# Performance work log

Hardware: AMD Instinct MI355X
Metric: run time of the kernel (lower is better)

## Reference

```python
import jax, jax.numpy as jnp
import numpy as np

B, S, E, H = 2, 2048, 1024, 16
D = E // H  # head_dim = 64


def setup_inputs() -> dict:
    key = jax.random.key(0)
    ks = jax.random.split(key, 6)
    scale = 1.0 / np.sqrt(E)
    x = jax.random.normal(ks[0], (B, S, E), dtype=jnp.float32)
    mask = jnp.ones((B, S), dtype=jnp.int32)
    Wqkv = jax.random.normal(ks[1], (E, 3 * E), dtype=jnp.float32) * scale
    bqkv = jax.random.normal(ks[2], (3 * E,), dtype=jnp.float32) * 0.01
    Wout = jax.random.normal(ks[3], (E, E), dtype=jnp.float32) * scale
    bout = jax.random.normal(ks[4], (E,), dtype=jnp.float32) * 0.01
    return {"x": x, "mask": mask, "Wqkv": Wqkv, "bqkv": bqkv, "Wout": Wout, "bout": bout}


def reference(x, mask, Wqkv, bqkv, Wout, bout):
    Bn, Sn, En = x.shape
    qkv = x @ Wqkv + bqkv                      # [B,S,3E]
    qkv = qkv.reshape(Bn, Sn, 3, H, D)
    qkv = jnp.transpose(qkv, (2, 0, 3, 1, 4))  # [3,B,H,S,D]
    q, k, v = qkv[0], qkv[1], qkv[2]
    scores = jnp.einsum('bhqd,bhkd->bhqk', q, k) / np.sqrt(D).astype(np.float32)
    m = mask[:, None, None, :]                 # [B,1,1,S]
    scores = jnp.where(m == 0, jnp.float32(-jnp.inf), scores)
    attn = jax.nn.softmax(scores, axis=-1)
    out = jnp.einsum('bhqk,bhkd->bhqd', attn, v)  # [B,H,S,D]
    out = jnp.transpose(out, (0, 2, 1, 3)).reshape(Bn, Sn, En)
    return out @ Wout + bout
```

## Files before the change

### kernel.cpp

```cpp
#include <hip/hip_runtime.h>


typedef __attribute__((ext_vector_type(8))) short short8;
typedef __attribute__((ext_vector_type(4))) short short4b;
typedef __attribute__((ext_vector_type(4))) float floatx4;
typedef __attribute__((ext_vector_type(16))) float floatx16;
typedef unsigned short ushort_t;

static __device__ __forceinline__ ushort_t f2bf(float f) {
    unsigned u = __float_as_uint(f);
    u += 0x7fffu + ((u >> 16) & 1u);
    return (ushort_t)(u >> 16);
}
static __device__ __forceinline__ float bf2f(ushort_t h) {
    return __uint_as_float(((unsigned)h) << 16);
}
#if __has_builtin(__builtin_amdgcn_cvt_pk_bf16_f32)
typedef __attribute__((ext_vector_type(2))) __bf16 bf16x2_t;
static __device__ __forceinline__ unsigned pack2bf(float a, float b) {
    bf16x2_t r = __builtin_amdgcn_cvt_pk_bf16_f32(a, b);
    return __builtin_bit_cast(unsigned, r);
}
#else
static __device__ __forceinline__ unsigned pack2bf(float a, float b) {
    return (unsigned)f2bf(a) | ((unsigned)f2bf(b) << 16);
}
#endif
static __device__ __forceinline__ float hexp2(float x) {
    return __builtin_amdgcn_exp2f(x);
}
static __device__ __forceinline__ void gload16(const void* g, void* l) {
    __builtin_amdgcn_global_load_lds(
        (const __attribute__((address_space(1))) unsigned int*)g,
        (__attribute__((address_space(3))) unsigned int*)l, 16, 0, 0);
}

#if __has_builtin(__builtin_amdgcn_permlane32_swap)
typedef __attribute__((ext_vector_type(2))) unsigned uint2v_t;
static __device__ __forceinline__ void plswap(unsigned x, unsigned y,
                                              unsigned& o0, unsigned& o1) {
    uint2v_t r = __builtin_amdgcn_permlane32_swap(x, y, false, false);
    o0 = r.x; o1 = r.y;
}
#else
static __device__ __forceinline__ void plswap(unsigned x, unsigned y,
                                              unsigned& o0, unsigned& o1) {
    int l = (int)(threadIdx.x & 63);
    bool hi = l >= 32;
    unsigned xsw = (unsigned)__shfl((int)x, l ^ 32);
    unsigned ysw = (unsigned)__shfl((int)y, l ^ 32);
    o0 = hi ? ysw : x;
    o1 = hi ? y : xsw;
}
#endif

__global__ __launch_bounds__(256) void prep(
    const float* __restrict__ x, ushort_t* __restrict__ xb,
    const float* __restrict__ Wqkv, ushort_t* __restrict__ wqT,
    const float* __restrict__ Wout, ushort_t* __restrict__ woT,
    const int* __restrict__ mask, float* __restrict__ maddg)
{
    __shared__ float tile[32][33];
    const int bk = blockIdx.x;
    const int t = threadIdx.x;
    if (bk < 4096) {
        int i = bk * 256 + t;
        float4 v = ((const float4*)x)[i];
        uint2 o;
        o.x = pack2bf(v.x, v.y);
        o.y = pack2bf(v.z, v.w);
        ((uint2*)xb)[i] = o;
        return;
    }
    if (bk < 8192) {
        const float* W; ushort_t* WT; int K, N, id;
        if (bk < 7168) { W = Wqkv; WT = wqT; K = 1024; N = 3072; id = bk - 4096;
                         int nb = (id % 96) * 32, kb = (id / 96) * 32;
                         const int r = t >> 3, c4 = (t & 7) * 4;
                         float4 v = *(const float4*)&W[(size_t)(kb + r) * N + nb + c4];
                         tile[r][c4+0]=v.x; tile[r][c4+1]=v.y; tile[r][c4+2]=v.z; tile[r][c4+3]=v.w;
                         __syncthreads();
                         uint2 o;
                         o.x = pack2bf(tile[c4+0][r], tile[c4+1][r]);
                         o.y = pack2bf(tile[c4+2][r], tile[c4+3][r]);
                         ((uint2*)WT)[((size_t)(nb + r) * K + kb + c4) >> 2] = o;
        } else {         W = Wout; WT = woT; K = 1024; N = 1024; id = bk - 7168;
                         int nb = (id % 32) * 32, kb = (id / 32) * 32;
                         const int r = t >> 3, c4 = (t & 7) * 4;
                         float4 v = *(const float4*)&W[(size_t)(kb + r) * N + nb + c4];
                         tile[r][c4+0]=v.x; tile[r][c4+1]=v.y; tile[r][c4+2]=v.z; tile[r][c4+3]=v.w;
                         __syncthreads();
                         uint2 o;
                         o.x = pack2bf(tile[c4+0][r], tile[c4+1][r]);
                         o.y = pack2bf(tile[c4+2][r], tile[c4+3][r]);
                         ((uint2*)WT)[((size_t)(nb + r) * K + kb + c4) >> 2] = o;
        }
        return;
    }
    {
        int i = (bk - 8192) * 256 + t;
        maddg[i] = (mask[i] ? 0.f : -1e30f) - 24.0f;
    }
}

__global__ __launch_bounds__(256, 3) void gemm_qkv(
    const ushort_t* __restrict__ A, const ushort_t* __restrict__ B,
    const float* __restrict__ bias, ushort_t* __restrict__ qkvb,
    ushort_t* __restrict__ vtg)
{
    const int K = 1024;
    __shared__ ushort_t Ah[128][32], Bh[128][32];
    __shared__ ushort_t Tb[64][136];
    const int bn = blockIdx.x * 128, bm = blockIdx.y * 128;
    const int t = threadIdx.x, w = t >> 6, lane = t & 63;
    const int l15 = lane & 15, quad = lane >> 4;
    const int wm = w >> 1, wn = w & 1;

    const int srow = w * 32 + (lane >> 2);
    const int skp  = (lane & 3) ^ ((lane >> 2) & 3);
    const int scol = skp * 8;
    const ushort_t* ga = A + (size_t)(bm + srow) * K + scol;
    const ushort_t* gb = B + (size_t)(bn + srow) * K + scol;
    const size_t rstep = (size_t)16 * K;
    const int fcol = ((quad ^ (l15 & 3)) * 8);

    floatx4 acc[4][4];
    #pragma unroll
    for (int mt = 0; mt < 4; ++mt)
        #pragma unroll
        for (int nt = 0; nt < 4; ++nt) acc[mt][nt] = (floatx4){0.f, 0.f, 0.f, 0.f};

    for (int k0 = 0; k0 < K; k0 += 32) {
        #pragma unroll
        for (int i = 0; i < 2; ++i) {
            gload16(ga + i * rstep + k0, &Ah[w * 32 + i * 16][0]);
            gload16(gb + i * rstep + k0, &Bh[w * 32 + i * 16][0]);
        }
        __syncthreads();
        short8 ah[4], bh[4];
        #pragma unroll
        for (int x = 0; x < 4; ++x) {
            ah[x] = *(const short8*)&Ah[wm * 64 + x * 16 + l15][fcol];
            bh[x] = *(const short8*)&Bh[wn * 64 + x * 16 + l15][fcol];
        }
        #pragma unroll
        for (int mt = 0; mt < 4; ++mt)
            #pragma unroll
            for (int nt = 0; nt < 4; ++nt)
                acc[mt][nt] = __builtin_amdgcn_mfma_f32_16x16x32_bf16(ah[mt], bh[nt], acc[mt][nt], 0, 0, 0);
        __syncthreads();
    }

    if (bn < 2048) {
        #pragma unroll
        for (int mt = 0; mt < 4; ++mt)
            #pragma unroll
            for (int r = 0; r < 4; ++r) {
                size_t row = (size_t)(bm + wm * 64 + mt * 16 + quad * 4 + r) * 2048;
                #pragma unroll
                for (int nt = 0; nt < 4; ++nt) {
                    int col = bn + wn * 64 + nt * 16 + l15;
                    qkvb[row + col] = f2bf(acc[mt][nt][r] + bias[col]);
                }
            }
    } else {
        const int h0 = (bn - 2048) >> 6;
        const int b  = bm >> 11, s0 = bm & 2047;
        #pragma unroll
        for (int hh = 0; hh < 2; ++hh) {
            if (wn == hh) {
                #pragma unroll
                for (int mt = 0; mt < 4; ++mt)
                    #pragma unroll
                    for (int nt = 0; nt < 4; ++nt) {
                        int d = nt * 16 + l15;
                        int sb = wm * 64 + mt * 16 + quad * 4;
                        float bv = bias[bn + hh * 64 + nt * 16 + l15];
                        uint2 pk;
                        pk.x = pack2bf(acc[mt][nt][0] + bv, acc[mt][nt][1] + bv);
                        pk.y = pack2bf(acc[mt][nt][2] + bv, acc[mt][nt][3] + bv);
                        *(uint2*)&Tb[d][sb] = pk;
                    }
            }
            __syncthreads();
            ushort_t* vbase = vtg + ((size_t)((b * 16 + h0 + hh) * 64)) * 2048 + s0;
            #pragma unroll
            for (int it = 0; it < 4; ++it) {
                int idx = t + it * 256;
                int d = idx >> 4, ch = idx & 15;
                uint4 v = *(const uint4*)&Tb[d][ch * 8];
                *(uint4*)&vbase[(size_t)d * 2048 + ch * 8] = v;
            }
            __syncthreads();
        }
    }
}

__global__ __launch_bounds__(256, 3) void gemm_bf16_f32_64(
    const ushort_t* __restrict__ A, const ushort_t* __restrict__ B,
    const float* __restrict__ bias, float* __restrict__ C,
    int M, int N, int K)
{
    __shared__ ushort_t Ah[64][32], Bh[128][32];
    const int bn = blockIdx.x * 128, bm = blockIdx.y * 64;
    const int t = threadIdx.x, w = t >> 6, lane = t & 63;
    const int l15 = lane & 15, quad = lane >> 4;
    const int wm = w >> 1, wn = w & 1;

    const int srow = w * 16 + (lane >> 2);
    const int skp  = (lane & 3) ^ ((lane >> 2) & 3);
    const int scol = skp * 8;
    const ushort_t* ga  = A + (size_t)(bm + srow) * K + scol;
    const ushort_t* gb0 = B + (size_t)(bn + srow) * K + scol;
    const ushort_t* gb1 = B + (size_t)(bn + 64 + srow) * K + scol;
    const int fcol = ((quad ^ (l15 & 3)) * 8);

    floatx4 acc[2][4];
    #pragma unroll
    for (int mt = 0; mt < 2; ++mt)
        #pragma unroll
        for (int nt = 0; nt < 4; ++nt) acc[mt][nt] = (floatx4){0.f, 0.f, 0.f, 0.f};

    for (int k0 = 0; k0 < K; k0 += 32) {
        gload16(ga  + k0, &Ah[w * 16][0]);
        gload16(gb0 + k0, &Bh[w * 16][0]);
        gload16(gb1 + k0, &Bh[64 + w * 16][0]);
        __syncthreads();
        short8 ah[2], bh[4];
        #pragma unroll
        for (int x = 0; x < 2; ++x)
            ah[x] = *(const short8*)&Ah[wm * 32 + x * 16 + l15][fcol];
        #pragma unroll
        for (int x = 0; x < 4; ++x)
            bh[x] = *(const short8*)&Bh[wn * 64 + x * 16 + l15][fcol];
        #pragma unroll
        for (int mt = 0; mt < 2; ++mt)
            #pragma unroll
            for (int nt = 0; nt < 4; ++nt)
                acc[mt][nt] = __builtin_amdgcn_mfma_f32_16x16x32_bf16(ah[mt], bh[nt], acc[mt][nt], 0, 0, 0);
        __syncthreads();
    }
    #pragma unroll
    for (int mt = 0; mt < 2; ++mt)
        #pragma unroll
        for (int r = 0; r < 4; ++r) {
            size_t row = (size_t)(bm + wm * 32 + mt * 16 + quad * 4 + r) * N;
            #pragma unroll
            for (int nt = 0; nt < 4; ++nt) {
                int col = bn + wn * 64 + nt * 16 + l15;
                C[row + col] = acc[mt][nt][r] + bias[col];
            }
        }
}

__global__ __launch_bounds__(512)
__attribute__((amdgpu_waves_per_eu(4, 4)))
void flash_v13(
    const ushort_t* __restrict__ qkv, const ushort_t* __restrict__ vtg,
    const float* __restrict__ maddg, ushort_t* __restrict__ attn)
{
    __shared__ __align__(16) ushort_t Ks[2][2][64][64];
    __shared__ __align__(16) ushort_t Vt[2][2][64][64];

    const int blk = blockIdx.x;
    const int xcd = blk & 7, rr = blk >> 3;
    const int qi = rr & 15, g = xcd + 8 * (rr >> 4);
    const int b = g >> 4, h = g & 15, q0 = qi * 128;

    const int t = threadIdx.x, wave = t >> 6, lane = t & 63;
    const int half = wave >> 2, wsub = wave & 3;
    const int l31 = lane & 31, hi = lane >> 5, l7 = lane & 7;
    const size_t bS = (size_t)b * 2048;
    const float c1 = 0.125f * 1.44269504088896340736f;

    short8 qf[4];
    {
        int q = q0 + wsub * 32 + l31;
        const ushort_t* qp = qkv + (bS + q) * 2048 + h * 64 + hi * 8;
        #pragma unroll
        for (int ks = 0; ks < 4; ++ks)
            qf[ks] = *(const short8*)(qp + ks * 16);
    }

    const int srow  = wsub * 16 + (lane >> 3);
    const int schnk = ((lane & 7) ^ ((lane >> 3) & 7)) * 8;
    const ushort_t* gK = qkv + (bS + half * 1024 + srow) * 2048 + 1024 + h * 64 + schnk;
    const ushort_t* gV = vtg + ((size_t)(b * 16 + h) * 64 + srow) * 2048 + half * 1024 + schnk;
    const float* gM = maddg + b * 2048 + half * 1024;

    auto stageK = [&](int buf, int kkt) {
        const ushort_t* p = gK + (size_t)(kkt * 64) * 2048;
        gload16(p,            &Ks[half][buf][wsub * 16][0]);
        gload16(p + 8 * 2048, &Ks[half][buf][wsub * 16 + 8][0]);
    };
    auto stageV = [&](int buf, int kkt) {
        gload16(gV + kkt * 64,            &Vt[half][buf][wsub * 16][0]);
        gload16(gV + kkt * 64 + 8 * 2048, &Vt[half][buf][wsub * 16 + 8][0]);
    };

    floatx16 outacc[2] = {};
    float lsum = 0.f;

    auto QKSM = [&](int kkt, int kb, unsigned (&Wd)[2][4][2]) {
        const int k0 = kkt * 64;
        #pragma unroll
        for (int t32 = 0; t32 < 2; ++t32) {
            floatx16 sc = {};
            __builtin_amdgcn_s_setprio(1);
            #pragma unroll
            for (int ks = 0; ks < 4; ++ks) {
                const int ch = ((2 * ks + hi) ^ l7) * 8;
                short8 ka = *(const short8*)&Ks[half][kb][t32 * 32 + l31][ch];
                sc = __builtin_amdgcn_mfma_f32_32x32x16_bf16(ka, qf[ks], sc, 0, 0, 0);
            }
            __builtin_amdgcn_s_setprio(0);
            #pragma unroll
            for (int gr = 0; gr < 4; ++gr) {
                float4 m4 = *(const float4*)&gM[k0 + t32 * 32 + gr * 8 + hi * 4];
                float p0 = hexp2(fmaf(sc[gr * 4 + 0], c1, m4.x));
                float p1 = hexp2(fmaf(sc[gr * 4 + 1], c1, m4.y));
                float p2 = hexp2(fmaf(sc[gr * 4 + 2], c1, m4.z));
                float p3 = hexp2(fmaf(sc[gr * 4 + 3], c1, m4.w));
                lsum += (p0 + p1) + (p2 + p3);
                Wd[t32][gr][0] = pack2bf(p0, p1);
                Wd[t32][gr][1] = pack2bf(p2, p3);
            }
        }
    };
    auto PV = [&](int vb, unsigned (&Wd)[2][4][2]) {
        #pragma unroll
        for (int ks2 = 0; ks2 < 4; ++ks2) {
            const int t32 = ks2 >> 1;
            const int ae  = (ks2 & 1) * 2;
            uint4 u;
            plswap(Wd[t32][ae][0], Wd[t32][ae + 1][0], u.x, u.z);
            plswap(Wd[t32][ae][1], Wd[t32][ae + 1][1], u.y, u.w);
            short8 pb = __builtin_bit_cast(short8, u);
            const int ch = ((2 * ks2 + hi) ^ l7) * 8;
            __builtin_amdgcn_s_setprio(1);
            #pragma unroll
            for (int dt = 0; dt < 2; ++dt) {
                short8 va = *(const short8*)&Vt[half][vb][dt * 32 + l31][ch];
                outacc[dt] = __builtin_amdgcn_mfma_f32_32x32x16_bf16(va, pb, outacc[dt], 0, 0, 0);
            }
            __builtin_amdgcn_s_setprio(0);
        }
    };

    stageK(0, 0);
    stageK(1, 1);
    stageV(0, 0);
    __syncthreads();
    unsigned Wc[2][4][2];
    QKSM(0, 0, Wc);
    __syncthreads();

    for (int kt = 0; kt < 16; ++kt) {
        if (kt + 2 < 16) stageK(kt & 1, kt + 2);
        if (kt + 1 < 16) stageV((kt + 1) & 1, kt + 1);
        unsigned Wn[2][4][2];
        if (kt + 1 < 16) QKSM(kt + 1, (kt + 1) & 1, Wn);
        PV(kt & 1, Wc);
        __syncthreads();
        if (kt + 1 < 16) {
            #pragma unroll
            for (int i = 0; i < 2; ++i)
                #pragma unroll
                for (int j = 0; j < 4; ++j) {
                    Wc[i][j][0] = Wn[i][j][0];
                    Wc[i][j][1] = Wn[i][j][1];
                }
        }
    }

    lsum += __shfl_xor(lsum, 32);

    float* Obuf = (float*)&Ks[0][0][0][0];
    float* Lbuf = (float*)&Vt[0][0][0][0];

    if (half == 1) {
        #pragma unroll
        for (int dt = 0; dt < 2; ++dt)
            #pragma unroll
            for (int i = 0; i < 16; ++i)
                Obuf[(wsub * 64 + lane) * 32 + ((dt * 16 + i) ^ l31)] = outacc[dt][i];
        Lbuf[wsub * 32 + l31] = lsum;
    }
    __syncthreads();
    if (half == 0) {
        float inv = 1.f / (lsum + Lbuf[wsub * 32 + l31]);
        int q = q0 + wsub * 32 + l31;
        ushort_t* orow = attn + (bS + q) * 1024 + h * 64;
        #pragma unroll
        for (int dt = 0; dt < 2; ++dt) {
            float o[16];
            #pragma unroll
            for (int i = 0; i < 16; ++i)
                o[i] = outacc[dt][i] + Obuf[(wsub * 64 + lane) * 32 + ((dt * 16 + i) ^ l31)];
            #pragma unroll
            for (int gr = 0; gr < 4; ++gr) {
                uint2 pk;
                pk.x = pack2bf(o[gr * 4 + 0] * inv, o[gr * 4 + 1] * inv);
                pk.y = pack2bf(o[gr * 4 + 2] * inv, o[gr * 4 + 3] * inv);
                *(uint2*)&orow[dt * 32 + gr * 8 + hi * 4] = pk;
            }
        }
    }
}

extern "C" void kernel_launch(void* const* d_in, const int* in_sizes, int n_in,
                              void* d_out, int out_size, void* d_ws, size_t ws_size,
                              hipStream_t stream) {
    const float* x    = (const float*)d_in[0];
    const int*   mask = (const int*)  d_in[1];
    const float* Wqkv = (const float*)d_in[2];
    const float* bqkv = (const float*)d_in[3];
    const float* Wout = (const float*)d_in[4];
    const float* bout = (const float*)d_in[5];
    float* out = (float*)d_out;

    char* ws = (char*)d_ws;
    ushort_t* xb    = (ushort_t*)(ws);
    ushort_t* wqT   = (ushort_t*)(ws + 8388608);
    ushort_t* qkvb  = (ushort_t*)(ws + 14680064);
    ushort_t* vtg   = (ushort_t*)(ws + 31457280);
    ushort_t* attnb = (ushort_t*)(ws + 39845888);
    ushort_t* woT   = (ushort_t*)(ws + 48234496);
    float*    maddg = (float*)   (ws + 50331648);

    const int M = 4096, E = 1024, N3 = 3072;

    prep<<<dim3(8208), dim3(256), 0, stream>>>(
        x, xb, Wqkv, wqT, Wout, woT, mask, maddg);

    gemm_qkv<<<dim3(N3 / 128, M / 128), dim3(256), 0, stream>>>(
        xb, wqT, bqkv, qkvb, vtg);

    flash_v13<<<dim3(512), dim3(512), 0, stream>>>(qkvb, vtg, maddg, attnb);

    gemm_bf16_f32_64<<<dim3(E / 128, M / 64), dim3(256), 0, stream>>>(
        attnb, woT, bout, out, M, E, E);
}
```

Baseline: 205.7 us.

## Interleave QK-softmax and PV at 32-key granularity with unrolled double-buffer loop

Splits the QK/softmax and PV stages into 32-key halves and interleaves them, so each PV MFMA pair is scheduled next to the next tile's QK MFMA work. The P fragments are packed into MFMA operands right after exponentiation, which removes the per-iteration register copy of the unnormalised weights. The main loop is unrolled by two with fixed buffer indices, removing modulo buffer selection. This may raise register pressure under the fixed waves-per-EU setting and only reshapes the flash kernel, which is one of four launches.

```diff
diff --git a/kernel.cpp b/kernel.cpp
--- a/kernel.cpp
+++ b/kernel.cpp
@@ -255,7 +255,7 @@
 
 __global__ __launch_bounds__(512)
 __attribute__((amdgpu_waves_per_eu(4, 4)))
-void flash_v13(
+void flash_v14(
     const ushort_t* __restrict__ qkv, const ushort_t* __restrict__ vtg,
     const float* __restrict__ maddg, ushort_t* __restrict__ attn)
 {
@@ -301,76 +301,79 @@
     floatx16 outacc[2] = {};
     float lsum = 0.f;
 
-    auto QKSM = [&](int kkt, int kb, unsigned (&Wd)[2][4][2]) {
+    auto QKSM32 = [&](int kkt, int t32, int kb, short8 (&PB)[2]) {
         const int k0 = kkt * 64;
-        #pragma unroll
-        for (int t32 = 0; t32 < 2; ++t32) {
-            floatx16 sc = {};
-            __builtin_amdgcn_s_setprio(1);
-            #pragma unroll
-            for (int ks = 0; ks < 4; ++ks) {
-                const int ch = ((2 * ks + hi) ^ l7) * 8;
-                short8 ka = *(const short8*)&Ks[half][kb][t32 * 32 + l31][ch];
-                sc = __builtin_amdgcn_mfma_f32_32x32x16_bf16(ka, qf[ks], sc, 0, 0, 0);
-            }
-            __builtin_amdgcn_s_setprio(0);
-            #pragma unroll
-            for (int gr = 0; gr < 4; ++gr) {
-                float4 m4 = *(const float4*)&gM[k0 + t32 * 32 + gr * 8 + hi * 4];
-                float p0 = hexp2(fmaf(sc[gr * 4 + 0], c1, m4.x));
-                float p1 = hexp2(fmaf(sc[gr * 4 + 1], c1, m4.y));
-                float p2 = hexp2(fmaf(sc[gr * 4 + 2], c1, m4.z));
-                float p3 = hexp2(fmaf(sc[gr * 4 + 3], c1, m4.w));
-                lsum += (p0 + p1) + (p2 + p3);
-                Wd[t32][gr][0] = pack2bf(p0, p1);
-                Wd[t32][gr][1] = pack2bf(p2, p3);
-            }
+        floatx16 sc = {};
+        __builtin_amdgcn_s_setprio(1);
+        #pragma unroll
+        for (int ks = 0; ks < 4; ++ks) {
+            const int ch = ((2 * ks + hi) ^ l7) * 8;
+            short8 ka = *(const short8*)&Ks[half][kb][t32 * 32 + l31][ch];
+            sc = __builtin_amdgcn_mfma_f32_32x32x16_bf16(ka, qf[ks], sc, 0, 0, 0);
+        }
+        __builtin_amdgcn_s_setprio(0);
+        unsigned Wt[4][2];
+        #pragma unroll
+        for (int gr = 0; gr < 4; ++gr) {
+            float4 m4 = *(const float4*)&gM[k0 + t32 * 32 + gr * 8 + hi * 4];
+            float p0 = hexp2(fmaf(sc[gr * 4 + 0], c1, m4.x));
+            float p1 = hexp2(fmaf(sc[gr * 4 + 1], c1, m4.y));
+            float p2 = hexp2(fmaf(sc[gr * 4 + 2], c1, m4.z));
+            float p3 = hexp2(fmaf(sc[gr * 4 + 3], c1, m4.w));
+            lsum += (p0 + p1) + (p2 + p3);
+            Wt[gr][0] = pack2bf(p0, p1);
+            Wt[gr][1] = pack2bf(p2, p3);
+        }
+        #pragma unroll
+        for (int kp = 0; kp < 2; ++kp) {
+            const int ae = kp * 2;
+            uint4 u;
+            plswap(Wt[ae][0], Wt[ae + 1][0], u.x, u.z);
+            plswap(Wt[ae][1], Wt[ae + 1][1], u.y, u.w);
+            PB[kp] = __builtin_bit_cast(short8, u);
         }
     };
-    auto PV = [&](int vb, unsigned (&Wd)[2][4][2]) {
-        #pragma unroll
-        for (int ks2 = 0; ks2 < 4; ++ks2) {
-            const int t32 = ks2 >> 1;
-            const int ae  = (ks2 & 1) * 2;
-            uint4 u;
-            plswap(Wd[t32][ae][0], Wd[t32][ae + 1][0], u.x, u.z);
-            plswap(Wd[t32][ae][1], Wd[t32][ae + 1][1], u.y, u.w);
-            short8 pb = __builtin_bit_cast(short8, u);
-            const int ch = ((2 * ks2 + hi) ^ l7) * 8;
+    auto PV32 = [&](int t32, int vb, short8 (&PB)[2]) {
+        #pragma unroll
+        for (int kp = 0; kp < 2; ++kp) {
+            const int ch = ((2 * (t32 * 2 + kp) + hi) ^ l7) * 8;
             __builtin_amdgcn_s_setprio(1);
             #pragma unroll
             for (int dt = 0; dt < 2; ++dt) {
                 short8 va = *(const short8*)&Vt[half][vb][dt * 32 + l31][ch];
-                outacc[dt] = __builtin_amdgcn_mfma_f32_32x32x16_bf16(va, pb, outacc[dt], 0, 0, 0);
+                outacc[dt] = __builtin_amdgcn_mfma_f32_32x32x16_bf16(va, PB[kp], outacc[dt], 0, 0, 0);
             }
             __builtin_amdgcn_s_setprio(0);
         }
     };
+
+    short8 PA0[2], PA1[2], PB0[2], PB1[2];
 
     stageK(0, 0);
     stageK(1, 1);
     stageV(0, 0);
     __syncthreads();
-    unsigned Wc[2][4][2];
-    QKSM(0, 0, Wc);
+    QKSM32(0, 0, 0, PA0);
+    QKSM32(0, 1, 0, PA1);
     __syncthreads();
 
-    for (int kt = 0; kt < 16; ++kt) {
-        if (kt + 2 < 16) stageK(kt & 1, kt + 2);
-        if (kt + 1 < 16) stageV((kt + 1) & 1, kt + 1);
-        unsigned Wn[2][4][2];
-        if (kt + 1 < 16) QKSM(kt + 1, (kt + 1) & 1, Wn);
-        PV(kt & 1, Wc);
-        __syncthreads();
-        if (kt + 1 < 16) {
-            #pragma unroll
-            for (int i = 0; i < 2; ++i)
-                #pragma unroll
-                for (int j = 0; j < 4; ++j) {
-                    Wc[i][j][0] = Wn[i][j][0];
-                    Wc[i][j][1] = Wn[i][j][1];
-                }
-        }
+    for (int kt = 0; kt < 16; kt += 2) {
+        if (kt + 2 < 16) stageK(0, kt + 2);
+        stageV(1, kt + 1);
+        QKSM32(kt + 1, 0, 1, PB0);
+        PV32(0, 0, PA0);
+        QKSM32(kt + 1, 1, 1, PB1);
+        PV32(1, 0, PA1);
+        __syncthreads();
+        if (kt + 3 < 16) stageK(1, kt + 3);
+        if (kt + 2 < 16) {
+            stageV(0, kt + 2);
+            QKSM32(kt + 2, 0, 0, PA0);
+        }
+        PV32(0, 1, PB0);
+        if (kt + 2 < 16) QKSM32(kt + 2, 1, 0, PA1);
+        PV32(1, 1, PB1);
+        __syncthreads();
     }
 
     lsum += __shfl_xor(lsum, 32);
@@ -436,7 +439,7 @@
     gemm_qkv<<<dim3(N3 / 128, M / 128), dim3(256), 0, stream>>>(
         xb, wqT, bqkv, qkvb, vtg);
 
-    flash_v13<<<dim3(512), dim3(512), 0, stream>>>(qkvb, vtg, maddg, attnb);
+    flash_v14<<<dim3(512), dim3(512), 0, stream>>>(qkvb, vtg, maddg, attnb);
 
     gemm_bf16_f32_64<<<dim3(E / 128, M / 64), dim3(256), 0, stream>>>(
         attnb, woT, bout, out, M, E, E);
```

Measured after the change: 243.7 us. 1.18x slower.
